# Kernel tuning notes

Hardware: AMD Instinct MI355X
Metric: run time of the kernel (lower is better)

## Reference

```python
import jax, jax.numpy as jnp
import numpy as np

NH = 8  # num_heads


def _conv1x1(w, b, x):
    # 1x1 conv == channel matmul: w [O,C], x [B,C,H,W]
    return jnp.einsum('oc,bchw->bohw', w, x) + b[None, :, None, None]


def _fwd(low_freq_feat, high_freq_feat, ext_context, road_feat,
         ext_proj_w, ext_proj_b, road_proj_w, road_proj_b,
         ext_qkv_w, ext_qkv_b, road_qkv_w, road_qkv_b,
         ext_out_w, ext_out_b, road_out_w, road_out_b,
         gate_ext_w, gate_ext_b, gate_road_w, gate_road_b):
    B, C, H, W = low_freq_feat.shape
    nh = NH
    hd = C // nh
    HW = H * W
    scale = hd ** -0.5

    ext_p = ext_context @ ext_proj_w.T + ext_proj_b          # [B,C]
    road_p = _conv1x1(road_proj_w, road_proj_b, road_feat)   # [B,C,H,W]

    eqkv = (ext_p @ ext_qkv_w.T + ext_qkv_b).reshape(B, 3, nh, hd)
    ext_q, ext_v = eqkv[:, 0], eqkv[:, 2]                    # [B,nh,hd]

    # torch: conv out [B,3C,H,W] viewed as (B,C,3,H,W) -> q/k/v interleaved over channels
    rqkv = _conv1x1(road_qkv_w, road_qkv_b, road_p).reshape(B, C, 3, H, W)
    road_k = rqkv[:, :, 1].reshape(B, nh, hd, HW).transpose(0, 1, 3, 2)  # [B,nh,HW,hd]
    road_v = rqkv[:, :, 2].reshape(B, nh, hd, HW).transpose(0, 1, 3, 2)

    # ext->road attention. The torch code expands ext_q to HW identical rows; one row
    # per (batch, head) gives a bit-identical result without the [B,nh,HW,HW] blowup.
    scores = jnp.einsum('bnd,bnpd->bnp', ext_q, road_k) * scale
    attn = jax.nn.softmax(scores, axis=-1)                   # [B,nh,HW]
    ext_head = jnp.einsum('bnp,bnpd->bnd', attn, road_v).reshape(B, C)
    ext_vec = ext_head @ ext_out_w.T + ext_out_b             # [B,C]
    ext_feat_spatial = jnp.broadcast_to(ext_vec[:, :, None, None], (B, C, H, W))

    # road->ext attention: all HW keys/values are copies of the single ext token, so
    # softmax is exactly uniform and the output per position is exactly ext_v. The
    # road_out 1x1 conv on a spatially-constant map is a single matvec per batch.
    road_vec = ext_v.reshape(B, C) @ road_out_w.T + road_out_b
    road_enhanced = jnp.broadcast_to(road_vec[:, :, None, None], (B, C, H, W))

    # gated fusion (ext stream): spatial mean of constant map == ext_vec
    gate_in = jnp.concatenate([low_freq_feat.mean(axis=(2, 3)), ext_vec], axis=-1)
    ext_gate = jax.nn.sigmoid(gate_in @ gate_ext_w.T + gate_ext_b)[:, :, None, None]
    ext_final = low_freq_feat * (1.0 - ext_gate) + ext_feat_spatial * ext_gate

    # gated fusion (road stream)
    rg_in = jnp.concatenate([high_freq_feat, road_enhanced], axis=1)  # [B,2C,H,W]
    road_gate = jax.nn.sigmoid(_conv1x1(gate_road_w, gate_road_b, rg_in))
    road_final = high_freq_feat * (1.0 - road_gate) + road_enhanced * road_gate
    return ext_final, road_final


def setup_inputs() -> dict:
    key = jax.random.key(0)
    ks = jax.random.split(key, 20)
    B, C, H, W, E = 8, 256, 64, 64, 64
    f = lambda k, shape, s=1.0: jax.random.normal(k, shape, dtype=jnp.float32) * s
    return {
        'low_freq_feat': f(ks[0], (B, C, H, W)),
        'high_freq_feat': f(ks[1], (B, C, H, W)),
        'ext_context': f(ks[2], (B, E)),
        'road_feat': f(ks[3], (B, C, H, W)),
        'ext_proj_w': f(ks[4], (C, E), 0.05), 'ext_proj_b': f(ks[5], (C,), 0.02),
        'road_proj_w': f(ks[6], (C, C), 0.05), 'road_proj_b': f(ks[7], (C,), 0.02),
        'ext_qkv_w': f(ks[8], (3 * C, C), 0.05), 'ext_qkv_b': f(ks[9], (3 * C,), 0.02),
        'road_qkv_w': f(ks[10], (3 * C, C), 0.05), 'road_qkv_b': f(ks[11], (3 * C,), 0.02),
        'ext_out_w': f(ks[12], (C, C), 0.05), 'ext_out_b': f(ks[13], (C,), 0.02),
        'road_out_w': f(ks[14], (C, C), 0.05), 'road_out_b': f(ks[15], (C,), 0.02),
        'gate_ext_w': f(ks[16], (C, 2 * C), 0.05), 'gate_ext_b': f(ks[17], (C,), 0.02),
        'gate_road_w': f(ks[18], (C, 2 * C), 0.05), 'gate_road_b': f(ks[19], (C,), 0.02),
    }


def reference(low_freq_feat, high_freq_feat, ext_context, road_feat,
              ext_proj_w, ext_proj_b, road_proj_w, road_proj_b,
              ext_qkv_w, ext_qkv_b, road_qkv_w, road_qkv_b,
              ext_out_w, ext_out_b, road_out_w, road_out_b,
              gate_ext_w, gate_ext_b, gate_road_w, gate_road_b):
    return _fwd(low_freq_feat, high_freq_feat, ext_context, road_feat,
                ext_proj_w, ext_proj_b, road_proj_w, road_proj_b,
                ext_qkv_w, ext_qkv_b, road_qkv_w, road_qkv_b,
                ext_out_w, ext_out_b, road_out_w, road_out_b,
                gate_ext_w, gate_ext_b, gate_road_w, gate_road_b)
```

## Files before the change

### kernel.cpp

```cpp
#include <hip/hip_runtime.h>

typedef short bf16x8 __attribute__((ext_vector_type(8)));
typedef float f32x4 __attribute__((ext_vector_type(4)));

__device__ __forceinline__ unsigned short f2b(float f) {
    unsigned int u = __builtin_bit_cast(unsigned int, f);
    unsigned int r = u + 0x7FFFu + ((u >> 16) & 1u);
    return (unsigned short)(r >> 16);
}

__global__ __launch_bounds__(256) void k_setup(const float* __restrict__ w1,
                                               const float* __restrict__ wqkv,
                                               const float* __restrict__ b1,
                                               const float* __restrict__ bqkv,
                                               const float* __restrict__ gate_road_w,
                                               const float* __restrict__ gate_road_b,
                                               const float* __restrict__ ext_context,
                                               const float* __restrict__ ext_proj_w,
                                               const float* __restrict__ ext_proj_b,
                                               const float* __restrict__ ext_qkv_w,
                                               const float* __restrict__ ext_qkv_b,
                                               const float* __restrict__ road_out_w,
                                               const float* __restrict__ road_out_b,
                                               unsigned short* __restrict__ W3b,
                                               unsigned short* __restrict__ Wcb,
                                               float* __restrict__ bcv,
                                               float* __restrict__ ext_q,
                                               float* __restrict__ road_vec,
                                               float* __restrict__ rg_const) {
    int bid = blockIdx.x, t = threadIdx.x;
    __shared__ float sel[8][256];
    __shared__ float red[8][4];
    if (bid < 256) {
        int i = bid * 256 + t;
        int o = i >> 8, k = i & 255;
        W3b[i] = f2b(gate_road_w[o * 512 + k]);
    } else if (bid < 320) {
        int o0 = (bid - 256) * 8;
        #pragma unroll
        for (int r = 0; r < 8; r++) {
            int o = o0 + r;
            int c = (o < 256) ? o : o - 256;
            int g = (o < 256) ? 1 : 2;
            sel[r][t] = wqkv[(size_t)(3 * c + g) * 256 + t];
        }
        __syncthreads();
        float b1v = b1[t];
        #pragma unroll
        for (int r = 0; r < 8; r++) {
            float v = sel[r][t] * b1v;
            for (int m = 32; m; m >>= 1) v += __shfl_xor(v, m, 64);
            if ((t & 63) == 0) red[r][t >> 6] = v;
        }
        __syncthreads();
        if (t < 8) {
            int o = o0 + t;
            int c = (o < 256) ? o : o - 256;
            int g = (o < 256) ? 1 : 2;
            bcv[o] = red[t][0] + red[t][1] + red[t][2] + red[t][3] + bqkv[3 * c + g];
        }
        float acc[8] = {};
        #pragma unroll 4
        for (int m = 0; m < 256; m++) {
            float w1v = w1[(size_t)m * 256 + t];
            #pragma unroll
            for (int r = 0; r < 8; r++) acc[r] += sel[r][m] * w1v;
        }
        #pragma unroll
        for (int r = 0; r < 8; r++) Wcb[(size_t)(o0 + r) * 256 + t] = f2b(acc[r]);
    } else {
        int b = bid - 320, c = t;
        float* ctx  = sel[0];
        float* extp = sel[1];
        float* extv = sel[2];
        float* rv   = sel[3];
        if (c < 64) ctx[c] = ext_context[b * 64 + c];
        __syncthreads();
        float s = ext_proj_b[c];
        #pragma unroll 4
        for (int k = 0; k < 64; k++) s += ext_proj_w[c * 64 + k] * ctx[k];
        extp[c] = s;
        __syncthreads();
        float q = ext_qkv_b[c], v = ext_qkv_b[512 + c];
        #pragma unroll 4
        for (int k = 0; k < 256; k++) {
            float p = extp[k];
            q += ext_qkv_w[c * 256 + k] * p;
            v += ext_qkv_w[(512 + c) * 256 + k] * p;
        }
        ext_q[b * 256 + c] = q;
        extv[c] = v;
        __syncthreads();
        float r = road_out_b[c];
        #pragma unroll 4
        for (int k = 0; k < 256; k++) r += road_out_w[c * 256 + k] * extv[k];
        road_vec[b * 256 + c] = r;
        rv[c] = r;
        __syncthreads();
        float g = gate_road_b[c];
        #pragma unroll 4
        for (int k = 0; k < 256; k++) g += gate_road_w[c * 512 + 256 + k] * rv[k];
        rg_const[b * 256 + c] = g;
    }
}

__global__ __launch_bounds__(256) void k_mean(const float* __restrict__ low,
                                              float* __restrict__ mean_low) {
    int bc = blockIdx.x, t = threadIdx.x;
    const f32x4* p4 = (const f32x4*)(low + (size_t)bc * 4096);
    float s = 0.f;
    for (int i = t; i < 1024; i += 256) {
        f32x4 v = p4[i];
        s += v[0] + v[1] + v[2] + v[3];
    }
    for (int m = 32; m; m >>= 1) s += __shfl_xor(s, m, 64);
    __shared__ float red[4];
    if ((t & 63) == 0) red[t >> 6] = s;
    __syncthreads();
    if (t == 0) mean_low[bc] = (red[0] + red[1] + red[2] + red[3]) * (1.0f / 4096.0f);
}

__global__ __launch_bounds__(512) void k_kv(const float* __restrict__ road_feat,
                                            const unsigned short* __restrict__ Wcb,
                                            const float* __restrict__ bcv,
                                            const float* __restrict__ extq,
                                            float* __restrict__ part) {
    __shared__ unsigned short Xs[64 * 256];
    __shared__ float esh[8][64];
    __shared__ float pvp[2][256];
    char* Xc = (char*)Xs;
    int bid = blockIdx.x;
    int b  = bid >> 6;
    int p0 = (bid & 63) << 6;
    int t  = threadIdx.x;
    const float* rfb = road_feat + (size_t)b * 1048576;

    int c0 = 2 * (t >> 4);
    int j4 = (t & 15) * 4;
    #pragma unroll
    for (int it = 0; it < 4; ++it) {
        int c = c0 + 64 * it;
        f32x4 g0 = *(const f32x4*)(rfb + (size_t)c * 4096 + p0 + j4);
        f32x4 g1 = *(const f32x4*)(rfb + (size_t)(c + 1) * 4096 + p0 + j4);
        #pragma unroll
        for (int i = 0; i < 4; i++) {
            int j = j4 + i;
            unsigned int pk = (unsigned int)f2b(g0[i]) | ((unsigned int)f2b(g1[i]) << 16);
            *(unsigned int*)(Xc + ((j * 512 + 2 * c) ^ ((j & 15) << 4))) = pk;
        }
    }
    __syncthreads();

    int w = t >> 6, lane = t & 63, l15 = lane & 15, lhi = lane >> 4;
    int wm = w >> 2, wn = w & 3;

    f32x4 acc[2][8] = {};
    for (int kk = 0; kk < 8; kk++) {
        bf16x8 a[2];
        #pragma unroll
        for (int mi = 0; mi < 2; mi++) {
            int j = wm * 32 + mi * 16 + l15;
            int off = (j * 512 + (kk * 32 + 8 * lhi) * 2) ^ ((j & 15) << 4);
            a[mi] = *(const bf16x8*)((const char*)Xs + off);
        }
        #pragma unroll
        for (int ni = 0; ni < 8; ni++) {
            int n = wn * 128 + ni * 16 + l15;
            bf16x8 bf = *(const bf16x8*)(Wcb + (size_t)n * 256 + kk * 32 + 8 * lhi);
            acc[0][ni] = __builtin_amdgcn_mfma_f32_16x16x32_bf16(a[0], bf, acc[0][ni], 0, 0, 0);
            acc[1][ni] = __builtin_amdgcn_mfma_f32_16x16x32_bf16(a[1], bf, acc[1][ni], 0, 0, 0);
        }
    }

    if (wn < 2) {
        float qA[4], qB[4], bk[8];
        #pragma unroll
        for (int hl = 0; hl < 4; ++hl) {
            int hg = wn * 4 + hl;
            qA[hl] = extq[b * 256 + hg * 32 + l15];
            qB[hl] = extq[b * 256 + hg * 32 + 16 + l15];
        }
        #pragma unroll
        for (int ni = 0; ni < 8; ni++) bk[ni] = bcv[wn * 128 + ni * 16 + l15];
        #pragma unroll
        for (int mi = 0; mi < 2; mi++)
            #pragma unroll
            for (int r = 0; r < 4; r++) {
                int j = wm * 32 + mi * 16 + 4 * lhi + r;
                #pragma unroll
                for (int hl = 0; hl < 4; hl++) {
                    float s = (acc[mi][2 * hl][r] + bk[2 * hl]) * qA[hl]
                            + (acc[mi][2 * hl + 1][r] + bk[2 * hl + 1]) * qB[hl];
                    s += __shfl_xor(s, 1, 64);
                    s += __shfl_xor(s, 2, 64);
                    s += __shfl_xor(s, 4, 64);
                    s += __shfl_xor(s, 8, 64);
                    if (l15 == 0)
                        esh[wn * 4 + hl][j] = expf(s * 0.17677669529663687f);
                }
            }
    }
    __syncthreads();

    float* pb = part + (size_t)bid * 264;
    if (wn >= 2) {
        #pragma unroll
        for (int ni = 0; ni < 8; ni++) {
            int cv = (wn - 2) * 128 + ni * 16 + l15;
            int hg = (wn - 2) * 4 + (ni >> 1);
            float bv = bcv[256 + cv];
            float p = 0.f;
            #pragma unroll
            for (int mi = 0; mi < 2; mi++)
                #pragma unroll
                for (int r = 0; r < 4; r++) {
                    int j = wm * 32 + mi * 16 + 4 * lhi + r;
                    p += esh[hg][j] * (acc[mi][ni][r] + bv);
                }
            p += __shfl_xor(p, 16, 64);
            p += __shfl_xor(p, 32, 64);
            if (lhi == 0) pvp[wm][cv] = p;
        }
    } else {
        int h0 = wn * 4 + wm * 2;
        float v0 = esh[h0][lane], v1 = esh[h0 + 1][lane];
        for (int m = 32; m; m >>= 1) {
            v0 += __shfl_xor(v0, m, 64);
            v1 += __shfl_xor(v1, m, 64);
        }
        if (lane == 0) { pb[h0] = v0; pb[h0 + 1] = v1; }
    }
    __syncthreads();
    if (t < 256) pb[8 + t] = pvp[0][t] + pvp[1][t];
}

__global__ __launch_bounds__(256) void k_vec(const float* __restrict__ part,
                                             const float* __restrict__ ext_out_w,
                                             const float* __restrict__ ext_out_b,
                                             const float* __restrict__ mean_low,
                                             const float* __restrict__ gate_ext_w,
                                             const float* __restrict__ gate_ext_b,
                                             float* __restrict__ ext_vec,
                                             float* __restrict__ ext_gate) {
    int b = blockIdx.x, c = threadIdx.x;
    __shared__ float hd_[256], ev[256], ml[256], tot[8];
    const float* pb = part + (size_t)b * 64 * 264;
    float a = 0.f;
    #pragma unroll 4
    for (int tile = 0; tile < 64; tile++) a += pb[tile * 264 + 8 + c];
    if (c < 8) {
        float s = 0.f;
        for (int tile = 0; tile < 64; tile++) s += pb[tile * 264 + c];
        tot[c] = 1.0f / s;
    }
    ml[c] = mean_low[b * 256 + c];
    __syncthreads();
    hd_[c] = a * tot[c >> 5];
    __syncthreads();
    float s = ext_out_b[c];
    #pragma unroll 4
    for (int k = 0; k < 256; k++) s += ext_out_w[c * 256 + k] * hd_[k];
    ext_vec[b * 256 + c] = s;
    ev[c] = s;
    __syncthreads();
    float z = gate_ext_b[c];
    #pragma unroll 4
    for (int k = 0; k < 256; k++)
        z += gate_ext_w[c * 512 + k] * ml[k] + gate_ext_w[c * 512 + 256 + k] * ev[k];
    ext_gate[b * 256 + c] = 1.0f / (1.0f + expf(-z));
}

__global__ __launch_bounds__(256) void k_ext_final(const float* __restrict__ low,
                                                   const float* __restrict__ ext_vec,
                                                   const float* __restrict__ ext_gate,
                                                   float* __restrict__ out) {
    int idx = blockIdx.x * 256 + threadIdx.x;
    #pragma unroll
    for (int rep = 0; rep < 4; ++rep) {
        int i = idx + rep * 524288;
        int bc = i >> 10;
        float g = ext_gate[bc];
        float vv = ext_vec[bc];
        f32x4 L = *(const f32x4*)(low + (size_t)i * 4);
        f32x4 o;
        #pragma unroll
        for (int c = 0; c < 4; c++) o[c] = L[c] + g * (vv - L[c]);
        *(f32x4*)(out + (size_t)i * 4) = o;
    }
}

__global__ __launch_bounds__(512) void k_road(const float* __restrict__ high,
                                              const unsigned short* __restrict__ W3b,
                                              const float* __restrict__ rg_const,
                                              const float* __restrict__ road_vec,
                                              float* __restrict__ outbuf) {
    __shared__ float Xs[64 * 256];
    char* Xc = (char*)Xs;
    int b  = blockIdx.x >> 6;
    int p0 = (blockIdx.x & 63) << 6;
    int t  = threadIdx.x;
    const float* hb = high + (size_t)b * 1048576;

    for (int it = 0; it < 8; ++it) {
        int c  = (t >> 4) + it * 32;
        int j4 = (t & 15) * 4;
        f32x4 g = *(const f32x4*)(hb + (size_t)c * 4096 + p0 + j4);
        #pragma unroll
        for (int i = 0; i < 4; i++) {
            int j = j4 + i;
            *(float*)(Xc + ((j * 1024 + 4 * c) ^ ((j & 15) << 4))) = g[i];
        }
    }
    __syncthreads();

    int w = t >> 6, lane = t & 63, l15 = lane & 15, lhi = lane >> 4;
    int wm = w >> 2, wn = w & 3;
    f32x4 acc[2][4] = {};
    for (int kk = 0; kk < 8; kk++) {
        bf16x8 a[2];
        #pragma unroll
        for (int mi = 0; mi < 2; mi++) {
            int j = wm * 32 + mi * 16 + l15;
            int base = j * 1024 + (kk * 32 + 8 * lhi) * 4;
            int sw = (j & 15) << 4;
            f32x4 x0 = *(const f32x4*)(Xc + (base ^ sw));
            f32x4 x1 = *(const f32x4*)(Xc + ((base + 16) ^ sw));
            bf16x8 av;
            #pragma unroll
            for (int i = 0; i < 4; i++) {
                av[i]     = (short)f2b(x0[i]);
                av[4 + i] = (short)f2b(x1[i]);
            }
            a[mi] = av;
        }
        #pragma unroll
        for (int ni = 0; ni < 4; ni++) {
            int o = wn * 64 + ni * 16 + l15;
            bf16x8 bf = *(const bf16x8*)(W3b + (size_t)o * 256 + kk * 32 + 8 * lhi);
            acc[0][ni] = __builtin_amdgcn_mfma_f32_16x16x32_bf16(a[0], bf, acc[0][ni], 0, 0, 0);
            acc[1][ni] = __builtin_amdgcn_mfma_f32_16x16x32_bf16(a[1], bf, acc[1][ni], 0, 0, 0);
        }
    }
    __syncthreads();

    #pragma unroll
    for (int ni = 0; ni < 4; ni++) {
        int o = wn * 64 + ni * 16 + l15;
        float rc = rg_const[b * 256 + o];
        float rv = road_vec[b * 256 + o];
        #pragma unroll
        for (int mi = 0; mi < 2; mi++)
            #pragma unroll
            for (int r = 0; r < 4; r++) {
                int j = wm * 32 + mi * 16 + 4 * lhi + r;
                float* slot = (float*)(Xc + ((j * 1024 + 4 * o) ^ ((j & 15) << 4)));
                float z = acc[mi][ni][r] + rc;
                float gte = 1.0f / (1.0f + expf(-z));
                float hv = *slot;
                *slot = hv + gte * (rv - hv);
            }
    }
    __syncthreads();

    float* ob = outbuf + 8388608 + (size_t)b * 1048576;
    for (int it = 0; it < 8; ++it) {
        int c  = (t >> 4) + it * 32;
        int j4 = (t & 15) * 4;
        f32x4 o4;
        #pragma unroll
        for (int i = 0; i < 4; i++) {
            int j = j4 + i;
            o4[i] = *(const float*)(Xc + ((j * 1024 + 4 * c) ^ ((j & 15) << 4)));
        }
        *(f32x4*)(ob + (size_t)c * 4096 + p0 + j4) = o4;
    }
}

extern "C" void kernel_launch(void* const* d_in, const int* in_sizes, int n_in,
                              void* d_out, int out_size, void* d_ws, size_t ws_size,
                              hipStream_t stream) {
    const float* low         = (const float*)d_in[0];
    const float* high        = (const float*)d_in[1];
    const float* ext_context = (const float*)d_in[2];
    const float* road_feat   = (const float*)d_in[3];
    const float* ext_proj_w  = (const float*)d_in[4];
    const float* ext_proj_b  = (const float*)d_in[5];
    const float* road_proj_w = (const float*)d_in[6];
    const float* road_proj_b = (const float*)d_in[7];
    const float* ext_qkv_w   = (const float*)d_in[8];
    const float* ext_qkv_b   = (const float*)d_in[9];
    const float* road_qkv_w  = (const float*)d_in[10];
    const float* road_qkv_b  = (const float*)d_in[11];
    const float* ext_out_w   = (const float*)d_in[12];
    const float* ext_out_b   = (const float*)d_in[13];
    const float* road_out_w  = (const float*)d_in[14];
    const float* road_out_b  = (const float*)d_in[15];
    const float* gate_ext_w  = (const float*)d_in[16];
    const float* gate_ext_b  = (const float*)d_in[17];
    const float* gate_road_w = (const float*)d_in[18];
    const float* gate_road_b = (const float*)d_in[19];

    float* out = (float*)d_out;
    unsigned short* wsb = (unsigned short*)d_ws;
    unsigned short* Wcb = wsb;
    unsigned short* W3b = wsb + 131072;
    float* fw = (float*)((char*)d_ws + 524288);
    float* ext_q    = fw;
    float* road_vec = fw + 2048;
    float* rg_const = fw + 4096;
    float* ext_vec  = fw + 8192;
    float* ext_gate = fw + 10240;
    float* mean_low = fw + 12288;
    float* bcv      = fw + 14336;
    float* part = out + 2097152;

    k_setup<<<328, 256, 0, stream>>>(road_proj_w, road_qkv_w, road_proj_b, road_qkv_b,
                                     gate_road_w, gate_road_b, ext_context,
                                     ext_proj_w, ext_proj_b, ext_qkv_w, ext_qkv_b,
                                     road_out_w, road_out_b,
                                     W3b, Wcb, bcv, ext_q, road_vec, rg_const);
    k_mean<<<2048, 256, 0, stream>>>(low, mean_low);
    k_kv<<<512, 512, 0, stream>>>(road_feat, Wcb, bcv, ext_q, part);
    k_vec<<<8, 256, 0, stream>>>(part, ext_out_w, ext_out_b, mean_low,
                                 gate_ext_w, gate_ext_b, ext_vec, ext_gate);
    k_ext_final<<<2048, 256, 0, stream>>>(low, ext_vec, ext_gate, out);
    k_road<<<512, 512, 0, stream>>>(high, W3b, rg_const, road_vec, out);
}
```

Measured before the change: 181.2 us.

## Halve spatial tile size in kv/road kernels and fold mean into setup

Reduces the spatial tile per block from 64 to 32 positions in k_kv and k_road, doubling grid size to 1024 blocks and shrinking LDS use so more blocks fit per CU. Warp roles are remapped so each wave covers a full 32-row tile, and the cross-wave partial reduction through shared memory is removed. The separate mean kernel is folded into k_setup as extra blocks, removing one launch. Each weight fragment is now reused across fewer rows, and k_vec has to sum twice as many partials.

```diff
diff --git a/kernel.cpp b/kernel.cpp
--- a/kernel.cpp
+++ b/kernel.cpp
@@ -22,16 +22,30 @@
                                                const float* __restrict__ ext_qkv_b,
                                                const float* __restrict__ road_out_w,
                                                const float* __restrict__ road_out_b,
+                                               const float* __restrict__ low,
                                                unsigned short* __restrict__ W3b,
                                                unsigned short* __restrict__ Wcb,
                                                float* __restrict__ bcv,
                                                float* __restrict__ ext_q,
                                                float* __restrict__ road_vec,
-                                               float* __restrict__ rg_const) {
+                                               float* __restrict__ rg_const,
+                                               float* __restrict__ mean_low) {
     int bid = blockIdx.x, t = threadIdx.x;
     __shared__ float sel[8][256];
     __shared__ float red[8][4];
-    if (bid < 256) {
+    if (bid >= 328) {
+        int bc = bid - 328;
+        const f32x4* p4 = (const f32x4*)(low + (size_t)bc * 4096);
+        float s = 0.f;
+        for (int i = t; i < 1024; i += 256) {
+            f32x4 v = p4[i];
+            s += v[0] + v[1] + v[2] + v[3];
+        }
+        for (int m = 32; m; m >>= 1) s += __shfl_xor(s, m, 64);
+        if ((t & 63) == 0) red[0][t >> 6] = s;
+        __syncthreads();
+        if (t == 0) mean_low[bc] = (red[0][0] + red[0][1] + red[0][2] + red[0][3]) * (1.0f / 4096.0f);
+    } else if (bid < 256) {
         int i = bid * 256 + t;
         int o = i >> 8, k = i & 255;
         W3b[i] = f2b(gate_road_w[o * 512 + k]);
@@ -104,42 +118,25 @@
     }
 }
 
-__global__ __launch_bounds__(256) void k_mean(const float* __restrict__ low,
-                                              float* __restrict__ mean_low) {
-    int bc = blockIdx.x, t = threadIdx.x;
-    const f32x4* p4 = (const f32x4*)(low + (size_t)bc * 4096);
-    float s = 0.f;
-    for (int i = t; i < 1024; i += 256) {
-        f32x4 v = p4[i];
-        s += v[0] + v[1] + v[2] + v[3];
-    }
-    for (int m = 32; m; m >>= 1) s += __shfl_xor(s, m, 64);
-    __shared__ float red[4];
-    if ((t & 63) == 0) red[t >> 6] = s;
-    __syncthreads();
-    if (t == 0) mean_low[bc] = (red[0] + red[1] + red[2] + red[3]) * (1.0f / 4096.0f);
-}
-
 __global__ __launch_bounds__(512) void k_kv(const float* __restrict__ road_feat,
                                             const unsigned short* __restrict__ Wcb,
                                             const float* __restrict__ bcv,
                                             const float* __restrict__ extq,
                                             float* __restrict__ part) {
-    __shared__ unsigned short Xs[64 * 256];
-    __shared__ float esh[8][64];
-    __shared__ float pvp[2][256];
+    __shared__ unsigned short Xs[32 * 256];
+    __shared__ float esh[8][32];
     char* Xc = (char*)Xs;
     int bid = blockIdx.x;
-    int b  = bid >> 6;
-    int p0 = (bid & 63) << 6;
+    int b  = bid >> 7;
+    int p0 = (bid & 127) << 5;
     int t  = threadIdx.x;
     const float* rfb = road_feat + (size_t)b * 1048576;
 
-    int c0 = 2 * (t >> 4);
-    int j4 = (t & 15) * 4;
+    int c0 = 2 * (t >> 3);
+    int j4 = (t & 7) * 4;
     #pragma unroll
-    for (int it = 0; it < 4; ++it) {
-        int c = c0 + 64 * it;
+    for (int it = 0; it < 2; ++it) {
+        int c = c0 + 128 * it;
         f32x4 g0 = *(const f32x4*)(rfb + (size_t)c * 4096 + p0 + j4);
         f32x4 g1 = *(const f32x4*)(rfb + (size_t)(c + 1) * 4096 + p0 + j4);
         #pragma unroll
@@ -152,86 +149,83 @@
     __syncthreads();
 
     int w = t >> 6, lane = t & 63, l15 = lane & 15, lhi = lane >> 4;
-    int wm = w >> 2, wn = w & 3;
-
-    f32x4 acc[2][8] = {};
+
+    f32x4 acc[2][4] = {};
     for (int kk = 0; kk < 8; kk++) {
         bf16x8 a[2];
         #pragma unroll
         for (int mi = 0; mi < 2; mi++) {
-            int j = wm * 32 + mi * 16 + l15;
+            int j = mi * 16 + l15;
             int off = (j * 512 + (kk * 32 + 8 * lhi) * 2) ^ ((j & 15) << 4);
             a[mi] = *(const bf16x8*)((const char*)Xs + off);
         }
         #pragma unroll
-        for (int ni = 0; ni < 8; ni++) {
-            int n = wn * 128 + ni * 16 + l15;
+        for (int ni = 0; ni < 4; ni++) {
+            int n = w * 64 + ni * 16 + l15;
             bf16x8 bf = *(const bf16x8*)(Wcb + (size_t)n * 256 + kk * 32 + 8 * lhi);
             acc[0][ni] = __builtin_amdgcn_mfma_f32_16x16x32_bf16(a[0], bf, acc[0][ni], 0, 0, 0);
             acc[1][ni] = __builtin_amdgcn_mfma_f32_16x16x32_bf16(a[1], bf, acc[1][ni], 0, 0, 0);
         }
     }
 
-    if (wn < 2) {
-        float qA[4], qB[4], bk[8];
-        #pragma unroll
-        for (int hl = 0; hl < 4; ++hl) {
-            int hg = wn * 4 + hl;
-            qA[hl] = extq[b * 256 + hg * 32 + l15];
-            qB[hl] = extq[b * 256 + hg * 32 + 16 + l15];
-        }
-        #pragma unroll
-        for (int ni = 0; ni < 8; ni++) bk[ni] = bcv[wn * 128 + ni * 16 + l15];
+    if (w < 4) {
+        float qv[4], bk[4];
+        #pragma unroll
+        for (int ni = 0; ni < 4; ni++) {
+            int n = w * 64 + ni * 16 + l15;
+            qv[ni] = extq[b * 256 + n];
+            bk[ni] = bcv[n];
+        }
         #pragma unroll
         for (int mi = 0; mi < 2; mi++)
             #pragma unroll
             for (int r = 0; r < 4; r++) {
-                int j = wm * 32 + mi * 16 + 4 * lhi + r;
+                int j = mi * 16 + 4 * lhi + r;
                 #pragma unroll
-                for (int hl = 0; hl < 4; hl++) {
-                    float s = (acc[mi][2 * hl][r] + bk[2 * hl]) * qA[hl]
-                            + (acc[mi][2 * hl + 1][r] + bk[2 * hl + 1]) * qB[hl];
+                for (int hl = 0; hl < 2; hl++) {
+                    float s = (acc[mi][2 * hl][r] + bk[2 * hl]) * qv[2 * hl]
+                            + (acc[mi][2 * hl + 1][r] + bk[2 * hl + 1]) * qv[2 * hl + 1];
                     s += __shfl_xor(s, 1, 64);
                     s += __shfl_xor(s, 2, 64);
                     s += __shfl_xor(s, 4, 64);
                     s += __shfl_xor(s, 8, 64);
                     if (l15 == 0)
-                        esh[wn * 4 + hl][j] = expf(s * 0.17677669529663687f);
+                        esh[w * 2 + hl][j] = expf(s * 0.17677669529663687f);
                 }
             }
     }
     __syncthreads();
 
     float* pb = part + (size_t)bid * 264;
-    if (wn >= 2) {
-        #pragma unroll
-        for (int ni = 0; ni < 8; ni++) {
-            int cv = (wn - 2) * 128 + ni * 16 + l15;
-            int hg = (wn - 2) * 4 + (ni >> 1);
+    if (w >= 4) {
+        #pragma unroll
+        for (int ni = 0; ni < 4; ni++) {
+            int cv = (w - 4) * 64 + ni * 16 + l15;
+            int hg = (w - 4) * 2 + (ni >> 1);
             float bv = bcv[256 + cv];
             float p = 0.f;
             #pragma unroll
             for (int mi = 0; mi < 2; mi++)
                 #pragma unroll
                 for (int r = 0; r < 4; r++) {
-                    int j = wm * 32 + mi * 16 + 4 * lhi + r;
+                    int j = mi * 16 + 4 * lhi + r;
                     p += esh[hg][j] * (acc[mi][ni][r] + bv);
                 }
             p += __shfl_xor(p, 16, 64);
             p += __shfl_xor(p, 32, 64);
-            if (lhi == 0) pvp[wm][cv] = p;
+            if (lhi == 0) pb[8 + cv] = p;
         }
     } else {
-        int h0 = wn * 4 + wm * 2;
-        float v0 = esh[h0][lane], v1 = esh[h0 + 1][lane];
-        for (int m = 32; m; m >>= 1) {
-            v0 += __shfl_xor(v0, m, 64);
-            v1 += __shfl_xor(v1, m, 64);
-        }
-        if (lane == 0) { pb[h0] = v0; pb[h0 + 1] = v1; }
-    }
-    __syncthreads();
-    if (t < 256) pb[8 + t] = pvp[0][t] + pvp[1][t];
+        int h0 = w * 2;
+        float v0 = (lane < 32) ? esh[h0][lane] : esh[h0 + 1][lane - 32];
+        v0 += __shfl_xor(v0, 1, 64);
+        v0 += __shfl_xor(v0, 2, 64);
+        v0 += __shfl_xor(v0, 4, 64);
+        v0 += __shfl_xor(v0, 8, 64);
+        v0 += __shfl_xor(v0, 16, 64);
+        if (lane == 0)  pb[h0] = v0;
+        if (lane == 32) pb[h0 + 1] = v0;
+    }
 }
 
 __global__ __launch_bounds__(256) void k_vec(const float* __restrict__ part,
@@ -244,13 +238,13 @@
                                              float* __restrict__ ext_gate) {
     int b = blockIdx.x, c = threadIdx.x;
     __shared__ float hd_[256], ev[256], ml[256], tot[8];
-    const float* pb = part + (size_t)b * 64 * 264;
+    const float* pb = part + (size_t)b * 128 * 264;
     float a = 0.f;
     #pragma unroll 4
-    for (int tile = 0; tile < 64; tile++) a += pb[tile * 264 + 8 + c];
+    for (int tile = 0; tile < 128; tile++) a += pb[tile * 264 + 8 + c];
     if (c < 8) {
         float s = 0.f;
-        for (int tile = 0; tile < 64; tile++) s += pb[tile * 264 + c];
+        for (int tile = 0; tile < 128; tile++) s += pb[tile * 264 + c];
         tot[c] = 1.0f / s;
     }
     ml[c] = mean_low[b * 256 + c];
@@ -294,16 +288,19 @@
                                               const float* __restrict__ rg_const,
                                               const float* __restrict__ road_vec,
                                               float* __restrict__ outbuf) {
-    __shared__ float Xs[64 * 256];
+    __shared__ float Xs[32 * 256];
     char* Xc = (char*)Xs;
-    int b  = blockIdx.x >> 6;
-    int p0 = (blockIdx.x & 63) << 6;
+    int bid = blockIdx.x;
+    int b  = bid >> 7;
+    int p0 = (bid & 127) << 5;
     int t  = threadIdx.x;
     const float* hb = high + (size_t)b * 1048576;
 
-    for (int it = 0; it < 8; ++it) {
-        int c  = (t >> 4) + it * 32;
-        int j4 = (t & 15) * 4;
+    int c0 = t >> 3;
+    int j4 = (t & 7) * 4;
+    #pragma unroll
+    for (int it = 0; it < 4; ++it) {
+        int c = c0 + 64 * it;
         f32x4 g = *(const f32x4*)(hb + (size_t)c * 4096 + p0 + j4);
         #pragma unroll
         for (int i = 0; i < 4; i++) {
@@ -314,13 +311,12 @@
     __syncthreads();
 
     int w = t >> 6, lane = t & 63, l15 = lane & 15, lhi = lane >> 4;
-    int wm = w >> 2, wn = w & 3;
-    f32x4 acc[2][4] = {};
+    f32x4 acc[2][2] = {};
     for (int kk = 0; kk < 8; kk++) {
         bf16x8 a[2];
         #pragma unroll
         for (int mi = 0; mi < 2; mi++) {
-            int j = wm * 32 + mi * 16 + l15;
+            int j = mi * 16 + l15;
             int base = j * 1024 + (kk * 32 + 8 * lhi) * 4;
             int sw = (j & 15) << 4;
             f32x4 x0 = *(const f32x4*)(Xc + (base ^ sw));
@@ -334,8 +330,8 @@
             a[mi] = av;
         }
         #pragma unroll
-        for (int ni = 0; ni < 4; ni++) {
-            int o = wn * 64 + ni * 16 + l15;
+        for (int ni = 0; ni < 2; ni++) {
+            int o = w * 32 + ni * 16 + l15;
             bf16x8 bf = *(const bf16x8*)(W3b + (size_t)o * 256 + kk * 32 + 8 * lhi);
             acc[0][ni] = __builtin_amdgcn_mfma_f32_16x16x32_bf16(a[0], bf, acc[0][ni], 0, 0, 0);
             acc[1][ni] = __builtin_amdgcn_mfma_f32_16x16x32_bf16(a[1], bf, acc[1][ni], 0, 0, 0);
@@ -344,15 +340,15 @@
     __syncthreads();
 
     #pragma unroll
-    for (int ni = 0; ni < 4; ni++) {
-        int o = wn * 64 + ni * 16 + l15;
+    for (int ni = 0; ni < 2; ni++) {
+        int o = w * 32 + ni * 16 + l15;
         float rc = rg_const[b * 256 + o];
         float rv = road_vec[b * 256 + o];
         #pragma unroll
         for (int mi = 0; mi < 2; mi++)
             #pragma unroll
             for (int r = 0; r < 4; r++) {
-                int j = wm * 32 + mi * 16 + 4 * lhi + r;
+                int j = mi * 16 + 4 * lhi + r;
                 float* slot = (float*)(Xc + ((j * 1024 + 4 * o) ^ ((j & 15) << 4)));
                 float z = acc[mi][ni][r] + rc;
                 float gte = 1.0f / (1.0f + expf(-z));
@@ -363,9 +359,9 @@
     __syncthreads();
 
     float* ob = outbuf + 8388608 + (size_t)b * 1048576;
-    for (int it = 0; it < 8; ++it) {
-        int c  = (t >> 4) + it * 32;
-        int j4 = (t & 15) * 4;
+    #pragma unroll
+    for (int it = 0; it < 4; ++it) {
+        int c = c0 + 64 * it;
         f32x4 o4;
         #pragma unroll
         for (int i = 0; i < 4; i++) {
@@ -414,15 +410,14 @@
     float* bcv      = fw + 14336;
     float* part = out + 2097152;
 
-    k_setup<<<328, 256, 0, stream>>>(road_proj_w, road_qkv_w, road_proj_b, road_qkv_b,
-                                     gate_road_w, gate_road_b, ext_context,
-                                     ext_proj_w, ext_proj_b, ext_qkv_w, ext_qkv_b,
-                                     road_out_w, road_out_b,
-                                     W3b, Wcb, bcv, ext_q, road_vec, rg_const);
-    k_mean<<<2048, 256, 0, stream>>>(low, mean_low);
-    k_kv<<<512, 512, 0, stream>>>(road_feat, Wcb, bcv, ext_q, part);
+    k_setup<<<2376, 256, 0, stream>>>(road_proj_w, road_qkv_w, road_proj_b, road_qkv_b,
+                                      gate_road_w, gate_road_b, ext_context,
+                                      ext_proj_w, ext_proj_b, ext_qkv_w, ext_qkv_b,
+                                      road_out_w, road_out_b, low,
+                                      W3b, Wcb, bcv, ext_q, road_vec, rg_const, mean_low);
+    k_kv<<<1024, 512, 0, stream>>>(road_feat, Wcb, bcv, ext_q, part);
     k_vec<<<8, 256, 0, stream>>>(part, ext_out_w, ext_out_b, mean_low,
                                  gate_ext_w, gate_ext_b, ext_vec, ext_gate);
     k_ext_final<<<2048, 256, 0, stream>>>(low, ext_vec, ext_gate, out);
-    k_road<<<512, 512, 0, stream>>>(high, W3b, rg_const, road_vec, out);
-}
+    k_road<<<1024, 512, 0, stream>>>(high, W3b, rg_const, road_vec, out);
+}
```

New measurement: 166.9 us. 7.8% less time.
